# Performance work log

Measured on AMD Instinct MI355X. Metric: run time of the kernel, lower is better.

Reference implementation:

```python
import jax, jax.numpy as jnp
import numpy as np

N = 100000
E = 1600000
NODE_DIM = 64
H = 128
NUM_LAYERS = 3
NUM_CLASSES = 6
NUM_GRAPHS = 512
LN_EPS = 1e-5


def setup_inputs() -> dict:
    key = jax.random.key(0)
    ks = jax.random.split(key, 16)
    s = 0.05
    x = jax.random.normal(ks[0], (N, NODE_DIM), jnp.float32)
    edge_index = jax.random.randint(ks[1], (2, E), 0, N, dtype=jnp.int64)
    batch = jnp.sort(jax.random.randint(ks[2], (N,), 0, NUM_GRAPHS, dtype=jnp.int64))
    return {
        "x": x,
        "edge_index": edge_index,
        "batch": batch,
        "proj_w": jax.random.normal(ks[3], (NODE_DIM, H), jnp.float32) * s,
        "proj_b": jnp.zeros((H,), jnp.float32),
        "lin_l_w": jax.random.normal(ks[4], (NUM_LAYERS, H, H), jnp.float32) * s,
        "lin_l_b": jnp.zeros((NUM_LAYERS, H), jnp.float32),
        "lin_r_w": jax.random.normal(ks[5], (NUM_LAYERS, H, H), jnp.float32) * s,
        "ln_g": jnp.ones((NUM_LAYERS, H), jnp.float32),
        "ln_b": jnp.zeros((NUM_LAYERS, H), jnp.float32),
        "gate_w1": jax.random.normal(ks[6], (H, H // 2), jnp.float32) * s,
        "gate_b1": jnp.zeros((H // 2,), jnp.float32),
        "gate_w2": jax.random.normal(ks[7], (H // 2, 1), jnp.float32) * s,
        "gate_b2": jnp.zeros((1,), jnp.float32),
        "cls_w1": jax.random.normal(ks[8], (H, H // 2), jnp.float32) * s,
        "cls_b1": jnp.zeros((H // 2,), jnp.float32),
        "cls_w2": jax.random.normal(ks[9], (H // 2, NUM_CLASSES), jnp.float32) * s,
        "cls_b2": jnp.zeros((NUM_CLASSES,), jnp.float32),
    }


def _layer_norm(x, g, b):
    mu = jnp.mean(x, axis=-1, keepdims=True)
    var = jnp.mean(jnp.square(x - mu), axis=-1, keepdims=True)
    return (x - mu) * jax.lax.rsqrt(var + LN_EPS) * g + b


def _sage_mean_aggr(x, src, dst):
    # mean of source node features grouped by destination node
    summed = jax.ops.segment_sum(x[src], dst, num_segments=N)  # [N,H]
    deg = jax.ops.segment_sum(jnp.ones((E,), x.dtype), dst, num_segments=N)
    return summed / jnp.maximum(deg, 1.0)[:, None]


def reference(x, edge_index, batch, proj_w, proj_b, lin_l_w, lin_l_b, lin_r_w,
              ln_g, ln_b, gate_w1, gate_b1, gate_w2, gate_b2,
              cls_w1, cls_b1, cls_w2, cls_b2):
    src, dst = edge_index[0], edge_index[1]
    h = jax.nn.relu(x @ proj_w + proj_b)  # [N,H]
    for l in range(NUM_LAYERS):
        r = h
        aggr = _sage_mean_aggr(h, src, dst)
        # PyG SAGEConv: lin_l(aggregated) + lin_r(self), bias only in lin_l
        h = aggr @ lin_l_w[l] + lin_l_b[l] + h @ lin_r_w[l]
        h = _layer_norm(h, ln_g[l], ln_b[l])
        h = jax.nn.elu(h)
        h = h + r  # dropout is identity in eval mode
    # GlobalAttention pooling: segment softmax over nodes per graph
    gate = (jax.nn.relu(h @ gate_w1 + gate_b1) @ gate_w2 + gate_b2)[:, 0]  # [N]
    gmax = jax.ops.segment_max(gate, batch, num_segments=NUM_GRAPHS)
    eg = jnp.exp(gate - gmax[batch])
    denom = jax.ops.segment_sum(eg, batch, num_segments=NUM_GRAPHS)
    alpha = eg / denom[batch]  # [N]
    pooled = jax.ops.segment_sum(h * alpha[:, None], batch, num_segments=NUM_GRAPHS)  # [G,H]
    out = jax.nn.relu(pooled @ cls_w1 + cls_b1) @ cls_w2 + cls_b2  # [G,C]
    return out
```

## Files before the change

### kernel.cpp

```cpp
#include <hip/hip_runtime.h>
#include <hip/hip_fp16.h>
#include <math.h>

#define N_NODES   100000
#define N_EDGES   1600000
#define NDIM      64
#define H         128
#define NUM_LAYERS 3
#define NUM_CLASSES 6
#define NUM_GRAPHS 512
#define LN_EPS    1e-5f
#define NBKT      391
#define SCAP      5376
#define BPAD      136

typedef _Float16 f16x8 __attribute__((ext_vector_type(8)));
typedef float    f32x4 __attribute__((ext_vector_type(4)));

__device__ __forceinline__ int idx_at(const int* raw, int is64, int i) {
    return is64 ? raw[2 * (long long)i] : raw[i];
}
__device__ __forceinline__ int lower_bound(const int* a, int n, int v) {
    int lo = 0, hi = n;
    while (lo < hi) { int m = (lo + hi) >> 1; if (a[m] < v) lo = m + 1; else hi = m; }
    return lo;
}

__device__ __forceinline__ f32x4 gload16(const __half* __restrict__ base, int voff) {
    f32x4 r;
    asm volatile("global_load_dwordx4 %0, %1, %2"
                 : "=v"(r) : "v"(voff), "s"(base));
    return r;
}

__global__ void k_detect(const int* eraw, const int* braw, int* flags) {
    if (threadIdx.x == 0 && blockIdx.x == 0) {
        int e64 = 1;
        for (int i = 1; i < 128; i += 2) if (eraw[i] != 0) { e64 = 0; break; }
        flags[0] = e64;
        flags[1] = (braw[N_NODES - 1] == 0) ? 1 : 0;
    }
}

__global__ void k_init(int* bcnt, float* gate_z) {
    int i = blockIdx.x * blockDim.x + threadIdx.x;
    if (i < 512) bcnt[i] = 0;
    if (i < 64) gate_z[i] = 0.f;
}

__global__ void k_conv_batch(const int* braw, const int* flags, int* batch32) {
    int i = blockIdx.x * blockDim.x + threadIdx.x;
    if (i < N_NODES) batch32[i] = idx_at(braw, flags[1], i);
}

__global__ __launch_bounds__(256) void k_bhist(const int* eraw, const int* flags, int* bcnt) {
    __shared__ int c[512];
    int tid = threadIdx.x;
    for (int i = tid; i < 512; i += 256) c[i] = 0;
    __syncthreads();
    int f = flags[0];
    int stride = gridDim.x * 256;
    for (int e = blockIdx.x * 256 + tid; e < N_EDGES; e += stride) {
        int d = idx_at(eraw, f, N_EDGES + e);
        atomicAdd(&c[d >> 8], 1);
    }
    __syncthreads();
    for (int i = tid; i < 512; i += 256) if (c[i]) atomicAdd(&bcnt[i], c[i]);
}

__global__ void k_bscan(const int* bcnt, int* boff, int* bcursor) {
    __shared__ int sh[512];
    int tid = threadIdx.x;
    int v = bcnt[tid];
    sh[tid] = v;
    __syncthreads();
    for (int off = 1; off < 512; off <<= 1) {
        int u = (tid >= off) ? sh[tid - off] : 0;
        __syncthreads();
        sh[tid] += u;
        __syncthreads();
    }
    int excl = sh[tid] - v;
    boff[tid] = excl;
    bcursor[tid] = excl;
    if (tid == 511) boff[512] = sh[511];
}

#define EPB 4096
__global__ __launch_bounds__(256) void k_bucket(const int* eraw, const int* flags,
                                                int* bcursor, unsigned int* br) {
    __shared__ int cnt[512];
    __shared__ int lcur[512];
    int tid = threadIdx.x;
    int f = flags[0];
    int base = blockIdx.x * EPB;
    int se[16], de[16];
#pragma unroll
    for (int j = 0; j < 16; ++j) {
        int e = base + j * 256 + tid;
        if (e < N_EDGES) {
            se[j] = idx_at(eraw, f, e);
            de[j] = idx_at(eraw, f, N_EDGES + e);
        } else de[j] = -1;
    }
    for (int i = tid; i < 512; i += 256) cnt[i] = 0;
    __syncthreads();
#pragma unroll
    for (int j = 0; j < 16; ++j)
        if (de[j] >= 0) atomicAdd(&cnt[de[j] >> 8], 1);
    __syncthreads();
    for (int i = tid; i < 512; i += 256)
        lcur[i] = cnt[i] ? atomicAdd(&bcursor[i], cnt[i]) : 0;
    __syncthreads();
#pragma unroll
    for (int j = 0; j < 16; ++j)
        if (de[j] >= 0) {
            int pos = atomicAdd(&lcur[de[j] >> 8], 1);
            br[pos] = ((unsigned int)(de[j] & 255) << 24) | (unsigned int)se[j];
        }
}

__global__ __launch_bounds__(256) void k_csr_tail(const unsigned int* br, const int* boff,
                                                  int* rowptr, int* col) {
    __shared__ int d256[256];
    __shared__ int sc[256];
    __shared__ int cbuf[SCAP];
    int b = blockIdx.x;
    int tid = threadIdx.x;
    int lo = boff[b], hi = boff[b + 1];
    int wsize = hi - lo;
    d256[tid] = 0;
    __syncthreads();
    for (int i = lo + tid; i < hi; i += 256)
        atomicAdd(&d256[br[i] >> 24], 1);
    __syncthreads();
    int v = d256[tid];
    sc[tid] = v;
    __syncthreads();
    for (int off = 1; off < 256; off <<= 1) {
        int u = (tid >= off) ? sc[tid - off] : 0;
        __syncthreads();
        sc[tid] += u;
        __syncthreads();
    }
    int excl = sc[tid] - v;
    int node = (b << 8) + tid;
    if (node < N_NODES) rowptr[node] = lo + excl;
    if (b == NBKT - 1 && tid == 0) rowptr[N_NODES] = N_EDGES;
    __syncthreads();
    d256[tid] = excl;
    __syncthreads();
    if (wsize <= SCAP) {
        for (int i = lo + tid; i < hi; i += 256) {
            unsigned int r = br[i];
            int p = atomicAdd(&d256[r >> 24], 1);
            cbuf[p] = (int)(r & 0xFFFFFF);
        }
        __syncthreads();
        for (int j = tid; j < wsize; j += 256) col[lo + j] = cbuf[j] << 8;
    } else {
        for (int i = lo + tid; i < hi; i += 256) {
            unsigned int r = br[i];
            int p = atomicAdd(&d256[r >> 24], 1);
            col[lo + p] = (int)(r & 0xFFFFFF) << 8;
        }
    }
}

__global__ void k_prepw(const float* __restrict__ lin_l_w, const float* __restrict__ lin_r_w,
                        const float* __restrict__ gate_w1,
                        __half* __restrict__ W16t, __half* __restrict__ W16g) {
    int i = blockIdx.x * 256 + threadIdx.x;
    if (i < NUM_LAYERS * 128 * 256) {
        int l = i >> 15;
        int rem = i & 32767;
        int n = rem >> 8;
        int k = rem & 255;
        float v = (k < 128) ? lin_l_w[(size_t)l * 16384 + k * 128 + n]
                            : lin_r_w[(size_t)l * 16384 + (k - 128) * 128 + n];
        W16t[(size_t)l * 32768 + n * 256 + k] = __float2half(v);
    } else if (i < NUM_LAYERS * 128 * 256 + 64 * 128) {
        int idx = i - NUM_LAYERS * 128 * 256;
        int n = idx >> 7;
        int k = idx & 127;
        W16g[n * 128 + k] = __float2half(gate_w1[k * 64 + n]);
    }
}

__global__ __launch_bounds__(256) void k_gemm_proj(const float* __restrict__ A,
                                                   const float* __restrict__ W,
                                                   const float* __restrict__ bias,
                                                   __half* __restrict__ C16,
                                                   int nrows, int K) {
    __shared__ float As_t[32][68];
    __shared__ float Ws[32 * 128];
    int tid = threadIdx.x;
    int row0 = blockIdx.x * 64;
    int tr = tid >> 4;
    int tc = tid & 15;
    int c0 = tc * 8;
    float acc[4][8];
#pragma unroll
    for (int i = 0; i < 4; ++i)
#pragma unroll
        for (int j = 0; j < 8; ++j) acc[i][j] = 0.f;

    for (int kc = 0; kc < K; kc += 32) {
        __syncthreads();
#pragma unroll
        for (int it = 0; it < 2; ++it) {
            int idx = tid + it * 256;
            int r = idx >> 3, c4 = idx & 7;
            int gr = row0 + r;
            float4 v = make_float4(0.f, 0.f, 0.f, 0.f);
            if (gr < nrows) v = *(const float4*)(A + (size_t)gr * K + kc + c4 * 4);
            As_t[c4 * 4 + 0][r] = v.x;
            As_t[c4 * 4 + 1][r] = v.y;
            As_t[c4 * 4 + 2][r] = v.z;
            As_t[c4 * 4 + 3][r] = v.w;
        }
#pragma unroll
        for (int it = 0; it < 4; ++it) {
            int idx = tid + it * 256;
            int r = idx >> 5, c4 = idx & 31;
            *(float4*)(&Ws[r * 128 + c4 * 4]) = *(const float4*)(W + (size_t)(kc + r) * 128 + c4 * 4);
        }
        __syncthreads();
#pragma unroll
        for (int k = 0; k < 32; ++k) {
            float4 a4 = *(const float4*)(&As_t[k][tr * 4]);
            float a[4] = {a4.x, a4.y, a4.z, a4.w};
            float4 w0 = *(const float4*)(&Ws[k * 128 + c0]);
            float4 w1 = *(const float4*)(&Ws[k * 128 + c0 + 4]);
            float w[8] = {w0.x, w0.y, w0.z, w0.w, w1.x, w1.y, w1.z, w1.w};
#pragma unroll
            for (int i = 0; i < 4; ++i)
#pragma unroll
                for (int j = 0; j < 8; ++j) acc[i][j] += a[i] * w[j];
        }
    }
    float bv[8];
#pragma unroll
    for (int j = 0; j < 8; ++j) bv[j] = bias[c0 + j];
#pragma unroll
    for (int i = 0; i < 4; ++i) {
        int gr = row0 + tr * 4 + i;
        if (gr < nrows) {
            float o[8];
#pragma unroll
            for (int j = 0; j < 8; ++j) o[j] = fmaxf(acc[i][j] + bv[j], 0.f);
            __half2 p[4];
#pragma unroll
            for (int j = 0; j < 8; j += 2) p[j / 2] = __floats2half2_rn(o[j], o[j + 1]);
            *(float4*)(C16 + (size_t)gr * 128 + c0) = *(float4*)p;
        }
    }
}

__global__ __launch_bounds__(256) void k_gate_mfma(const __half* __restrict__ h16,
                                                   const __half* __restrict__ W16g,
                                                   const float* __restrict__ b1,
                                                   const float* __restrict__ w2,
                                                   const float* __restrict__ b2,
                                                   float* __restrict__ gate) {
    __shared__ __half Bs[64 * BPAD];
    int tid = threadIdx.x;
    int wave = tid >> 6, lane = tid & 63;
    int s = lane & 15, quad = lane >> 4;
    int row0 = blockIdx.x * 64 + wave * 16;
    int arow = row0 + s;
    if (arow >= N_NODES) arow = N_NODES - 1;

#pragma unroll
    for (int it = 0; it < 4; ++it) {
        int idx = tid + it * 256;
        int n = idx >> 4, ch = idx & 15;
        *(float4*)(&Bs[n * BPAD + ch * 8]) = *(const float4*)(W16g + (size_t)n * 128 + ch * 8);
    }
    __syncthreads();

    f32x4 acc[4];
#pragma unroll
    for (int c = 0; c < 4; ++c) acc[c] = (f32x4){0.f, 0.f, 0.f, 0.f};

    const __half* aptr = h16 + (size_t)arow * H;
#pragma unroll
    for (int kc = 0; kc < 128; kc += 32) {
        f16x8 afrag = *(const f16x8*)(aptr + kc + quad * 8);
#pragma unroll
        for (int c = 0; c < 4; ++c) {
            f16x8 bfrag = *(const f16x8*)(&Bs[(c * 16 + s) * BPAD + kc + quad * 8]);
            acc[c] = __builtin_amdgcn_mfma_f32_16x16x32_f16(afrag, bfrag, acc[c], 0, 0, 0);
        }
    }
    float part[4] = {0.f, 0.f, 0.f, 0.f};
#pragma unroll
    for (int c = 0; c < 4; ++c) {
        float bv = b1[c * 16 + s];
        float wv = w2[c * 16 + s];
#pragma unroll
        for (int i = 0; i < 4; ++i)
            part[i] += fmaxf(acc[c][i] + bv, 0.f) * wv;
    }
#pragma unroll
    for (int off = 1; off < 16; off <<= 1) {
#pragma unroll
        for (int i = 0; i < 4; ++i) part[i] += __shfl_xor(part[i], off);
    }
    if (s == 0) {
        float b2v = b2[0];
#pragma unroll
        for (int i = 0; i < 4; ++i) {
            int r = row0 + quad * 4 + i;
            if (r < N_NODES) gate[r] = part[i] + b2v;
        }
    }
}

__global__ __launch_bounds__(64) void k_softmax_g(float* __restrict__ gate,
                                                  const int* __restrict__ batch32,
                                                  float* __restrict__ gsum) {
    int g = blockIdx.x;
    int lane = threadIdx.x;
    int n0 = lower_bound(batch32, N_NODES, g);
    int n1 = lower_bound(batch32, N_NODES, g + 1);
    float m = -INFINITY;
    for (int n = n0 + lane; n < n1; n += 64) m = fmaxf(m, gate[n]);
#pragma unroll
    for (int off = 32; off >= 1; off >>= 1) m = fmaxf(m, __shfl_xor(m, off));
    float s = 0.f;
    for (int n = n0 + lane; n < n1; n += 64) {
        float e = expf(gate[n] - m);
        gate[n] = e;
        s += e;
    }
#pragma unroll
    for (int off = 32; off >= 1; off >>= 1) s += __shfl_xor(s, off);
    if (lane == 0) gsum[g] = s;
}

__global__ __launch_bounds__(256) void k_pool_g(const __half* __restrict__ h16,
                                                const float* __restrict__ eg,
                                                const float* __restrict__ gsum,
                                                const int* __restrict__ batch32,
                                                float* __restrict__ pooled) {
    __shared__ float sacc[256];
    int g = blockIdx.x;
    int tid = threadIdx.x;
    int c = tid & 127;
    int p = tid >> 7;
    int n0 = lower_bound(batch32, N_NODES, g);
    int n1 = lower_bound(batch32, N_NODES, g + 1);
    float acc = 0.f;
    for (int n = n0 + p; n < n1; n += 2)
        acc += eg[n] * __half2float(h16[(size_t)n * H + c]);
    sacc[tid] = acc;
    __syncthreads();
    if (tid < 128) {
        float s = gsum[g];
        float v = sacc[tid] + sacc[tid + 128];
        pooled[(size_t)g * H + tid] = (n1 > n0) ? v / s : 0.f;
    }
}

__global__ __launch_bounds__(256) void k_layer_mfma(const __half* __restrict__ t16,
                                                    __half* __restrict__ h16,
                                                    const __half* __restrict__ W16t,
                                                    const float* __restrict__ bl,
                                                    const float* __restrict__ g,
                                                    const float* __restrict__ bb) {
    __shared__ __half Bs[128 * BPAD];
    int tid = threadIdx.x;
    int wave = tid >> 6, lane = tid & 63;
    int s = lane & 15, quad = lane >> 4;
    int row0 = blockIdx.x * 64;
    int wrow0 = row0 + wave * 16;
    int arow = wrow0 + s;
    if (arow >= N_NODES) arow = N_NODES - 1;

    f32x4 acc[8];
#pragma unroll
    for (int c = 0; c < 8; ++c) acc[c] = (f32x4){0.f, 0.f, 0.f, 0.f};

#pragma unroll
    for (int ph = 0; ph < 2; ++ph) {
        __syncthreads();
#pragma unroll
        for (int it = 0; it < 8; ++it) {
            int idx = tid + it * 256;
            int n = idx >> 4, ch = idx & 15;
            *(float4*)(&Bs[n * BPAD + ch * 8]) =
                *(const float4*)(W16t + (size_t)n * 256 + ph * 128 + ch * 8);
        }
        __syncthreads();
        const __half* aptr = (ph ? h16 : t16) + (size_t)arow * H;
#pragma unroll
        for (int kk = 0; kk < 128; kk += 32) {
            f16x8 afrag = *(const f16x8*)(aptr + kk + quad * 8);
#pragma unroll
            for (int c = 0; c < 8; ++c) {
                f16x8 bfrag = *(const f16x8*)(&Bs[(c * 16 + s) * BPAD + kk + quad * 8]);
                acc[c] = __builtin_amdgcn_mfma_f32_16x16x32_f16(afrag, bfrag, acc[c], 0, 0, 0);
            }
        }
    }

    float y[8][4];
    float sm[4] = {0.f, 0.f, 0.f, 0.f}, sq[4] = {0.f, 0.f, 0.f, 0.f};
#pragma unroll
    for (int c = 0; c < 8; ++c) {
        float bv = bl[c * 16 + s];
#pragma unroll
        for (int i = 0; i < 4; ++i) {
            float v = acc[c][i] + bv;
            y[c][i] = v;
            sm[i] += v;
            sq[i] += v * v;
        }
    }
#pragma unroll
    for (int off = 1; off < 16; off <<= 1) {
#pragma unroll
        for (int i = 0; i < 4; ++i) {
            sm[i] += __shfl_xor(sm[i], off);
            sq[i] += __shfl_xor(sq[i], off);
        }
    }
    float mean[4], rstd[4];
#pragma unroll
    for (int i = 0; i < 4; ++i) {
        mean[i] = sm[i] * (1.0f / H);
        float var = sq[i] * (1.0f / H) - mean[i] * mean[i];
        rstd[i] = rsqrtf(var + LN_EPS);
    }
    float gv[8], bbv[8];
#pragma unroll
    for (int c = 0; c < 8; ++c) { gv[c] = g[c * 16 + s]; bbv[c] = bb[c * 16 + s]; }

    __syncthreads();
#pragma unroll
    for (int i = 0; i < 4; ++i) {
        int lr = wave * 16 + quad * 4 + i;
#pragma unroll
        for (int c = 0; c < 8; ++c) {
            float yv = (y[c][i] - mean[i]) * rstd[i] * gv[c] + bbv[c];
            yv = yv > 0.f ? yv : expf(yv) - 1.f;
            Bs[lr * BPAD + c * 16 + s] = __float2half(yv);
        }
    }
    __syncthreads();
#pragma unroll
    for (int it = 0; it < 4; ++it) {
        int idx = tid + it * 256;
        int r = idx >> 4, ch = idx & 15;
        int grow = row0 + r;
        if (grow < N_NODES) {
            float4 sv = *(float4*)(&Bs[r * BPAD + ch * 8]);
            float4 hv = *(const float4*)(h16 + (size_t)grow * H + ch * 8);
            __half2* pa = (__half2*)&sv;
            const __half2* pb = (const __half2*)&hv;
#pragma unroll
            for (int j = 0; j < 4; ++j) {
                float2 fa = __half22float2(pa[j]);
                float2 fb = __half22float2(pb[j]);
                pa[j] = __floats2half2_rn(fa.x + fb.x, fa.y + fb.y);
            }
            *(float4*)(h16 + (size_t)grow * H + ch * 8) = sv;
        }
    }
}

__global__ __launch_bounds__(256) void k_aggr(const __half* __restrict__ h16,
                                              const int* __restrict__ rowptr,
                                              const int* __restrict__ col,
                                              __half* __restrict__ t16,
                                              int zoff) {
    int lane = threadIdx.x & 63;
    int node = blockIdx.x * 4 + (threadIdx.x >> 6);
    if (node >= N_NODES) return;
    int s = lane & 15;
    int g = lane >> 4;
    int soff = s * 16;
    int e0 = rowptr[node];
    int deg = rowptr[node + 1] - e0;

    if (deg == 0) {
        if (g == 0) {
            float4 zz = make_float4(0.f, 0.f, 0.f, 0.f);
            *(float4*)(t16 + (size_t)node * H + s * 8) = zz;
        }
        return;
    }

    __half2 z = __floats2half2_rn(0.f, 0.f);
    __half2 ac[4][4];
#pragma unroll
    for (int a = 0; a < 4; ++a)
#pragma unroll
        for (int k = 0; k < 4; ++k) ac[a][k] = z;

    {
        int cb[8];
#pragma unroll
        for (int j = 0; j < 8; ++j) {
            int ei = g + 4 * j;
            cb[j] = col[e0 + (ei < deg ? ei : 0)];
        }
#pragma unroll
        for (int j = 0; j < 8; ++j) {
            int ei = g + 4 * j;
            cb[j] = (ei < deg) ? cb[j] : zoff;
        }
        f32x4 rv[8];
#pragma unroll
        for (int j = 0; j < 8; ++j) rv[j] = gload16(h16, cb[j] + soff);
        asm volatile("s_waitcnt vmcnt(0)" ::: "memory");
        __builtin_amdgcn_sched_barrier(0);
#pragma unroll
        for (int j = 0; j < 8; ++j) {
            const __half2* hv = (const __half2*)&rv[j];
            int a = j & 3;
            ac[a][0] = __hadd2(ac[a][0], hv[0]);
            ac[a][1] = __hadd2(ac[a][1], hv[1]);
            ac[a][2] = __hadd2(ac[a][2], hv[2]);
            ac[a][3] = __hadd2(ac[a][3], hv[3]);
        }
    }

    if (deg > 32) {
        for (int base = 32; base < deg; base += 32) {
            int cb[8];
#pragma unroll
            for (int j = 0; j < 8; ++j) {
                int ei = base + g + 4 * j;
                cb[j] = col[e0 + (ei < deg ? ei : base)];
            }
#pragma unroll
            for (int j = 0; j < 8; ++j) {
                int ei = base + g + 4 * j;
                cb[j] = (ei < deg) ? cb[j] : zoff;
            }
            f32x4 rv[8];
#pragma unroll
            for (int j = 0; j < 8; ++j) rv[j] = gload16(h16, cb[j] + soff);
            asm volatile("s_waitcnt vmcnt(0)" ::: "memory");
            __builtin_amdgcn_sched_barrier(0);
#pragma unroll
            for (int j = 0; j < 8; ++j) {
                const __half2* hv = (const __half2*)&rv[j];
                int a = j & 3;
                ac[a][0] = __hadd2(ac[a][0], hv[0]);
                ac[a][1] = __hadd2(ac[a][1], hv[1]);
                ac[a][2] = __hadd2(ac[a][2], hv[2]);
                ac[a][3] = __hadd2(ac[a][3], hv[3]);
            }
        }
    }

    float f[8];
#pragma unroll
    for (int k = 0; k < 4; ++k) {
        float2 s0 = __half22float2(ac[0][k]);
        float2 s1 = __half22float2(ac[1][k]);
        float2 s2 = __half22float2(ac[2][k]);
        float2 s3 = __half22float2(ac[3][k]);
        f[2 * k]     = (s0.x + s1.x) + (s2.x + s3.x);
        f[2 * k + 1] = (s0.y + s1.y) + (s2.y + s3.y);
    }
#pragma unroll
    for (int off = 16; off <= 32; off <<= 1) {
#pragma unroll
        for (int k = 0; k < 8; ++k) f[k] += __shfl_xor(f[k], off);
    }
    if (g == 0) {
        float inv = 1.0f / (float)(deg > 1 ? deg : 1);
        __half2 o[4];
#pragma unroll
        for (int k = 0; k < 4; ++k)
            o[k] = __floats2half2_rn(f[2 * k] * inv, f[2 * k + 1] * inv);
        *(float4*)(t16 + (size_t)node * H + s * 8) = *(float4*)o;
    }
}

__global__ __launch_bounds__(64) void k_cls(const float* __restrict__ pooled,
                                            const float* __restrict__ w1,
                                            const float* __restrict__ b1,
                                            const float* __restrict__ w2,
                                            const float* __restrict__ b2,
                                            float* __restrict__ out) {
    __shared__ float sp[64];
    int g = blockIdx.x;
    int lane = threadIdx.x;
    float r0 = pooled[(size_t)g * H + lane];
    float r1 = pooled[(size_t)g * H + 64 + lane];
    float acc = b1[lane];
#pragma unroll 16
    for (int k = 0; k < 64; ++k) acc += __shfl(r0, k) * w1[k * 64 + lane];
#pragma unroll 16
    for (int k = 0; k < 64; ++k) acc += __shfl(r1, k) * w1[(64 + k) * 64 + lane];
    sp[lane] = fmaxf(acc, 0.f);
    __syncthreads();
    if (lane < NUM_CLASSES) {
        float o = b2[lane];
        for (int c = 0; c < 64; ++c) o += sp[c] * w2[c * NUM_CLASSES + lane];
        out[g * NUM_CLASSES + lane] = o;
    }
}

extern "C" void kernel_launch(void* const* d_in, const int* in_sizes, int n_in,
                              void* d_out, int out_size, void* d_ws, size_t ws_size,
                              hipStream_t stream) {
    const float* x       = (const float*)d_in[0];
    const int*   eraw    = (const int*)d_in[1];
    const int*   braw    = (const int*)d_in[2];
    const float* proj_w  = (const float*)d_in[3];
    const float* proj_b  = (const float*)d_in[4];
    const float* lin_l_w = (const float*)d_in[5];
    const float* lin_l_b = (const float*)d_in[6];
    const float* lin_r_w = (const float*)d_in[7];
    const float* ln_g    = (const float*)d_in[8];
    const float* ln_b    = (const float*)d_in[9];
    const float* gate_w1 = (const float*)d_in[10];
    const float* gate_b1 = (const float*)d_in[11];
    const float* gate_w2 = (const float*)d_in[12];
    const float* gate_b2 = (const float*)d_in[13];
    const float* cls_w1  = (const float*)d_in[14];
    const float* cls_b1  = (const float*)d_in[15];
    const float* cls_w2  = (const float*)d_in[16];
    const float* cls_b2  = (const float*)d_in[17];
    float* out = (float*)d_out;

    __half* h16    = (__half*)d_ws;
    __half* t16    = h16 + (size_t)N_NODES * H;
    float*  gate   = (float*)(t16 + (size_t)N_NODES * H);
    float*  gsum   = gate + N_NODES;
    float*  pooled = gsum + NUM_GRAPHS;
    __half* W16t   = (__half*)(pooled + NUM_GRAPHS * H);
    __half* W16g   = W16t + (size_t)NUM_LAYERS * 32768;
    int* flags     = (int*)(W16g + 64 * 128);
    int* col       = flags + 4;
    int* batch32   = col + N_EDGES;
    int* rowptr    = batch32 + N_NODES;
    int* bcnt      = rowptr + N_NODES + 1;
    int* boff      = bcnt + 512;
    int* bcursor   = boff + 513;
    unsigned int* br = (unsigned int*)(bcursor + 512);

    const int zoff = (int)((const char*)gate - (const char*)h16);

    const int nbN = (N_NODES + 255) / 256;
    const int nbE4 = (N_EDGES + EPB - 1) / EPB;
    const int nbW = (N_NODES + 3) / 4;
    const int nbG = (N_NODES + 63) / 64;
    const int nbP = (NUM_LAYERS * 128 * 256 + 64 * 128 + 255) / 256;

    k_detect<<<1, 1, 0, stream>>>(eraw, braw, flags);
    k_init<<<2, 256, 0, stream>>>(bcnt, gate);
    k_conv_batch<<<nbN, 256, 0, stream>>>(braw, flags, batch32);
    k_bhist<<<512, 256, 0, stream>>>(eraw, flags, bcnt);
    k_bscan<<<1, 512, 0, stream>>>(bcnt, boff, bcursor);
    k_bucket<<<nbE4, 256, 0, stream>>>(eraw, flags, bcursor, br);
    k_csr_tail<<<NBKT, 256, 0, stream>>>(br, boff, rowptr, col);
    k_prepw<<<nbP, 256, 0, stream>>>(lin_l_w, lin_r_w, gate_w1, W16t, W16g);

    k_gemm_proj<<<nbG, 256, 0, stream>>>(x, proj_w, proj_b, h16, N_NODES, NDIM);

    for (int l = 0; l < NUM_LAYERS; ++l) {
        const float* bl  = lin_l_b + (size_t)l * H;
        const float* gl  = ln_g + (size_t)l * H;
        const float* blb = ln_b + (size_t)l * H;
        k_aggr<<<nbW, 256, 0, stream>>>(h16, rowptr, col, t16, zoff);
        k_layer_mfma<<<nbG, 256, 0, stream>>>(t16, h16, W16t + (size_t)l * 32768, bl, gl, blb);
    }

    k_gate_mfma<<<nbG, 256, 0, stream>>>(h16, W16g, gate_b1, gate_w2, gate_b2, gate);
    k_softmax_g<<<NUM_GRAPHS, 64, 0, stream>>>(gate, batch32, gsum);
    k_pool_g<<<NUM_GRAPHS, 256, 0, stream>>>(h16, gate, gsum, batch32, pooled);
    k_cls<<<NUM_GRAPHS, 64, 0, stream>>>(pooled, cls_w1, cls_b1, cls_w2, cls_b2, out);
}
```

Measured before the change: 480.4 us.

## Stage bucketed edges in shared memory, merge init kernels, vectorize pooling

The bucket kernel now sorts each block's edges by bucket in shared memory and then writes them to the global bucket array in contiguous runs, replacing scattered per-edge global stores. The detect and init kernels are merged into one launch. The pooling kernel reads half2 pairs with four node lanes per channel pair instead of single halves. The aggregation precomputes its offsets before a scheduling barrier. This adds shared memory and an extra scan to the bucket kernel, which may lower its occupancy.

```diff
diff --git a/kernel.cpp b/kernel.cpp
--- a/kernel.cpp
+++ b/kernel.cpp
@@ -33,19 +33,17 @@
     return r;
 }
 
-__global__ void k_detect(const int* eraw, const int* braw, int* flags) {
-    if (threadIdx.x == 0 && blockIdx.x == 0) {
-        int e64 = 1;
-        for (int i = 1; i < 128; i += 2) if (eraw[i] != 0) { e64 = 0; break; }
-        flags[0] = e64;
-        flags[1] = (braw[N_NODES - 1] == 0) ? 1 : 0;
-    }
-}
-
-__global__ void k_init(int* bcnt, float* gate_z) {
+__global__ void k_detect(const int* eraw, const int* braw, int* flags,
+                         int* bcnt, float* gate_z) {
     int i = blockIdx.x * blockDim.x + threadIdx.x;
     if (i < 512) bcnt[i] = 0;
     if (i < 64) gate_z[i] = 0.f;
+    if (i == 0) {
+        int e64 = 1;
+        for (int k = 1; k < 128; k += 2) if (eraw[k] != 0) { e64 = 0; break; }
+        flags[0] = e64;
+        flags[1] = (braw[N_NODES - 1] == 0) ? 1 : 0;
+    }
 }
 
 __global__ void k_conv_batch(const int* braw, const int* flags, int* batch32) {
@@ -90,7 +88,12 @@
 __global__ __launch_bounds__(256) void k_bucket(const int* eraw, const int* flags,
                                                 int* bcursor, unsigned int* br) {
     __shared__ int cnt[512];
+    __shared__ int excl[512];
+    __shared__ int resv[512];
     __shared__ int lcur[512];
+    __shared__ int psum[256];
+    __shared__ unsigned int srec[EPB];
+    __shared__ unsigned short sbkt[EPB];
     int tid = threadIdx.x;
     int f = flags[0];
     int base = blockIdx.x * EPB;
@@ -109,15 +112,37 @@
     for (int j = 0; j < 16; ++j)
         if (de[j] >= 0) atomicAdd(&cnt[de[j] >> 8], 1);
     __syncthreads();
-    for (int i = tid; i < 512; i += 256)
-        lcur[i] = cnt[i] ? atomicAdd(&bcursor[i], cnt[i]) : 0;
+    int b0 = cnt[2 * tid], b1 = cnt[2 * tid + 1];
+    psum[tid] = b0 + b1;
+    __syncthreads();
+    for (int off = 1; off < 256; off <<= 1) {
+        int u = (tid >= off) ? psum[tid - off] : 0;
+        __syncthreads();
+        psum[tid] += u;
+        __syncthreads();
+    }
+    int pex = psum[tid] - (b0 + b1);
+    excl[2 * tid] = pex;
+    excl[2 * tid + 1] = pex + b0;
+    lcur[2 * tid] = pex;
+    lcur[2 * tid + 1] = pex + b0;
+    resv[2 * tid]     = b0 ? atomicAdd(&bcursor[2 * tid], b0) : 0;
+    resv[2 * tid + 1] = b1 ? atomicAdd(&bcursor[2 * tid + 1], b1) : 0;
     __syncthreads();
 #pragma unroll
     for (int j = 0; j < 16; ++j)
         if (de[j] >= 0) {
-            int pos = atomicAdd(&lcur[de[j] >> 8], 1);
-            br[pos] = ((unsigned int)(de[j] & 255) << 24) | (unsigned int)se[j];
-        }
+            int b = de[j] >> 8;
+            int slot = atomicAdd(&lcur[b], 1);
+            srec[slot] = ((unsigned int)(de[j] & 255) << 24) | (unsigned int)se[j];
+            sbkt[slot] = (unsigned short)b;
+        }
+    __syncthreads();
+    int vtot = psum[255];
+    for (int s2 = tid; s2 < vtot; s2 += 256) {
+        int b = sbkt[s2];
+        br[resv[b] + (s2 - excl[b])] = srec[s2];
+    }
 }
 
 __global__ __launch_bounds__(256) void k_csr_tail(const unsigned int* br, const int* boff,
@@ -344,22 +369,31 @@
                                                 const float* __restrict__ gsum,
                                                 const int* __restrict__ batch32,
                                                 float* __restrict__ pooled) {
-    __shared__ float sacc[256];
+    __shared__ float sx[256], sy[256];
     int g = blockIdx.x;
     int tid = threadIdx.x;
-    int c = tid & 127;
-    int p = tid >> 7;
+    int c2 = tid & 63;
+    int p = tid >> 6;
     int n0 = lower_bound(batch32, N_NODES, g);
     int n1 = lower_bound(batch32, N_NODES, g + 1);
-    float acc = 0.f;
-    for (int n = n0 + p; n < n1; n += 2)
-        acc += eg[n] * __half2float(h16[(size_t)n * H + c]);
-    sacc[tid] = acc;
-    __syncthreads();
-    if (tid < 128) {
+    float ax = 0.f, ay = 0.f;
+    for (int n = n0 + p; n < n1; n += 4) {
+        __half2 v = *(const __half2*)(h16 + (size_t)n * H + c2 * 2);
+        float2 fv = __half22float2(v);
+        float w = eg[n];
+        ax += w * fv.x;
+        ay += w * fv.y;
+    }
+    sx[tid] = ax; sy[tid] = ay;
+    __syncthreads();
+    if (tid < 64) {
         float s = gsum[g];
-        float v = sacc[tid] + sacc[tid + 128];
-        pooled[(size_t)g * H + tid] = (n1 > n0) ? v / s : 0.f;
+        float vx = sx[tid] + sx[tid + 64] + sx[tid + 128] + sx[tid + 192];
+        float vy = sy[tid] + sy[tid + 64] + sy[tid + 128] + sy[tid + 192];
+        float2 o;
+        o.x = (n1 > n0) ? vx / s : 0.f;
+        o.y = (n1 > n0) ? vy / s : 0.f;
+        *(float2*)(pooled + (size_t)g * H + c2 * 2) = o;
     }
 }
 
@@ -509,11 +543,12 @@
 #pragma unroll
         for (int j = 0; j < 8; ++j) {
             int ei = g + 4 * j;
-            cb[j] = (ei < deg) ? cb[j] : zoff;
-        }
+            cb[j] = ((ei < deg) ? cb[j] : zoff) + soff;
+        }
+        __builtin_amdgcn_sched_barrier(0);
         f32x4 rv[8];
 #pragma unroll
-        for (int j = 0; j < 8; ++j) rv[j] = gload16(h16, cb[j] + soff);
+        for (int j = 0; j < 8; ++j) rv[j] = gload16(h16, cb[j]);
         asm volatile("s_waitcnt vmcnt(0)" ::: "memory");
         __builtin_amdgcn_sched_barrier(0);
 #pragma unroll
@@ -538,11 +573,12 @@
 #pragma unroll
             for (int j = 0; j < 8; ++j) {
                 int ei = base + g + 4 * j;
-                cb[j] = (ei < deg) ? cb[j] : zoff;
+                cb[j] = ((ei < deg) ? cb[j] : zoff) + soff;
             }
+            __builtin_amdgcn_sched_barrier(0);
             f32x4 rv[8];
 #pragma unroll
-            for (int j = 0; j < 8; ++j) rv[j] = gload16(h16, cb[j] + soff);
+            for (int j = 0; j < 8; ++j) rv[j] = gload16(h16, cb[j]);
             asm volatile("s_waitcnt vmcnt(0)" ::: "memory");
             __builtin_amdgcn_sched_barrier(0);
 #pragma unroll
@@ -654,8 +690,7 @@
     const int nbG = (N_NODES + 63) / 64;
     const int nbP = (NUM_LAYERS * 128 * 256 + 64 * 128 + 255) / 256;
 
-    k_detect<<<1, 1, 0, stream>>>(eraw, braw, flags);
-    k_init<<<2, 256, 0, stream>>>(bcnt, gate);
+    k_detect<<<2, 256, 0, stream>>>(eraw, braw, flags, bcnt, gate);
     k_conv_batch<<<nbN, 256, 0, stream>>>(braw, flags, batch32);
     k_bhist<<<512, 256, 0, stream>>>(eraw, flags, bcnt);
     k_bscan<<<1, 512, 0, stream>>>(bcnt, boff, bcursor);
```

Measured after the change: 475.5 us. Within noise of the previous version (-1.0%).
